# Optimization experiments

Hardware: AMD Instinct MI355X
Metric: run time of the kernel (lower is better)

The kernel has to match this reference:

```python
import jax, jax.numpy as jnp
from jax import lax
import numpy as np

B, T, H, I, O = 256, 2048, 150, 1, 1

def setup_inputs() -> dict:
    key = jax.random.key(0)
    ks = jax.random.split(key, 7)
    s = 1.0 / np.sqrt(H)
    return {
        "input": jax.random.normal(ks[0], (B, T), dtype=jnp.float32),
        "W_ih": jax.random.uniform(ks[1], (3 * H, I), jnp.float32, -s, s),
        "W_hh": jax.random.uniform(ks[2], (3 * H, H), jnp.float32, -s, s),
        "b_ih": jax.random.uniform(ks[3], (3 * H,), jnp.float32, -s, s),
        "b_hh": jax.random.uniform(ks[4], (3 * H,), jnp.float32, -s, s),
        "W_lin": jax.random.uniform(ks[5], (O, H), jnp.float32, -s, s),
        "b_lin": jax.random.uniform(ks[6], (O,), jnp.float32, -s, s),
    }

def reference(input, W_ih, W_hh, b_ih, b_hh, W_lin, b_lin):
    # input: [B, T]; GRUCell recurrence with relu on hidden, per-step linear head.
    hidden = W_hh.shape[1]

    def step(h, x_t):  # h: [B, H], x_t: [B, 1]
        gi = x_t @ W_ih.T + b_ih          # [B, 3H]
        gh = h @ W_hh.T + b_hh            # [B, 3H]
        i_r, i_z, i_n = jnp.split(gi, 3, axis=-1)
        h_r, h_z, h_n = jnp.split(gh, 3, axis=-1)
        r = jax.nn.sigmoid(i_r + h_r)
        z = jax.nn.sigmoid(i_z + h_z)
        n = jnp.tanh(i_n + r * h_n)
        h_new = jax.nn.relu((1.0 - z) * n + z * h)  # relu applied as in original
        y = h_new @ W_lin.T + b_lin       # [B, 1]
        return h_new, y

    xs = jnp.transpose(input)[:, :, None]            # [T, B, 1]
    h0 = jnp.zeros((input.shape[0], hidden), input.dtype)
    _, ys = lax.scan(step, h0, xs)                   # ys: [T, B, 1]
    return jnp.transpose(ys[:, :, 0])                # [B, T] (stack dim=1, squeeze(2))
```

## Files before the change

### kernel.cpp

```cpp
#include <hip/hip_runtime.h>
#include <math.h>


#define BB 256
#define TT 2048
#define HH 150
#define H3 450

typedef float fx2 __attribute__((ext_vector_type(2)));

#define WCLOB \
  "v100","v101","v102","v103","v104","v105","v106","v107","v108","v109", \
  "v110","v111","v112","v113","v114","v115","v116","v117","v118","v119", \
  "v120","v121","v122","v123","v124","v125","v126","v127","v128","v129", \
  "v130","v131","v132","v133","v134","v135","v136","v137","v138","v139", \
  "v140","v141","v142","v143","v144","v145","v146","v147","v148","v149", \
  "v150","v151","v152","v153","v154","v155","v156","v157","v158","v159", \
  "v160","v161","v162","v163","v164","v165","v166","v167","v168","v169", \
  "v170","v171","v172","v173","v174","v175","v176","v177","v178","v179", \
  "v180","v181","v182","v183","v184","v185","v186","v187","v188","v189", \
  "v190","v191","v192","v193","v194","v195","v196","v197","v198","v199", \
  "v200","v201","v202","v203","v204","v205","v206","v207","v208","v209", \
  "v210","v211","v212","v213","v214","v215","v216","v217","v218","v219", \
  "v220","v221","v222","v223","v224","v225","v226","v227","v228","v229", \
  "v230","v231","v232","v233","v234","v235","v236","v237","v238","v239", \
  "v240","v241","v242","v243","v244","v245","v246","v247","v248","v249", \
  "v250","v251"

#define LD8(a0,a1,b0,b1,c0,c1,d0,d1,OFF) \
  "global_load_dword v" #a0 ", %[p0], off offset:" #OFF "\n\t" \
  "global_load_dword v" #a1 ", %[p1], off offset:" #OFF "\n\t" \
  "global_load_dword v" #b0 ", %[p2], off offset:" #OFF "\n\t" \
  "global_load_dword v" #b1 ", %[p3], off offset:" #OFF "\n\t" \
  "global_load_dword v" #c0 ", %[p4], off offset:" #OFF "\n\t" \
  "global_load_dword v" #c1 ", %[p5], off offset:" #OFF "\n\t" \
  "global_load_dword v" #d0 ", %[p6], off offset:" #OFF "\n\t" \
  "global_load_dword v" #d1 ", %[p7], off offset:" #OFF "\n\t"

#define PKB(sp, vp, acc) \
  "v_pk_fma_f32 " acc ", " sp ", " vp ", " acc " op_sel:[0,0,0] op_sel_hi:[0,1,1]\n\t"

#define G4(m0,m1,m2,m3, A0,B0,C0,D0, A1,B1,C1,D1, A2,B2,C2,D2, A3,B3,C3,D3) \
  "v_readlane_b32 s20, %[hq], " #m0 "\n\t" \
  "v_readlane_b32 s22, %[hq], " #m1 "\n\t" \
  "v_readlane_b32 s24, %[hq], " #m2 "\n\t" \
  "v_readlane_b32 s26, %[hq], " #m3 "\n\t" \
  PKB("s[20:21]", A0, "%[a01]") PKB("s[20:21]", B0, "%[a23]") \
  PKB("s[20:21]", C0, "%[a45]") PKB("s[20:21]", D0, "%[a67]") \
  PKB("s[22:23]", A1, "%[a01]") PKB("s[22:23]", B1, "%[a23]") \
  PKB("s[22:23]", C1, "%[a45]") PKB("s[22:23]", D1, "%[a67]") \
  PKB("s[24:25]", A2, "%[a01]") PKB("s[24:25]", B2, "%[a23]") \
  PKB("s[24:25]", C2, "%[a45]") PKB("s[24:25]", D2, "%[a67]") \
  PKB("s[26:27]", A3, "%[a01]") PKB("s[26:27]", B3, "%[a23]") \
  PKB("s[26:27]", C3, "%[a45]") PKB("s[26:27]", D3, "%[a67]")

__global__ __launch_bounds__(512, 2) void gru_seq_kernel(
    const float* __restrict__ input,
    const float* __restrict__ W_ih,
    const float* __restrict__ W_hh,
    const float* __restrict__ b_ih,
    const float* __restrict__ b_hh,
    const float* __restrict__ W_lin,
    const float* __restrict__ b_lin,
    float* __restrict__ out)
{
    const int b    = blockIdx.x;
    const int tid  = threadIdx.x;
    const int lane = tid & 63;
    const int wid  = tid >> 6;

    __shared__ float xrow[TT];
    __shared__ float PPf[4160];
    __shared__ float hb[520];
    __shared__ float yout[TT];

    ((float4*)xrow)[tid] = ((const float4*)(input + (size_t)b * TT))[tid];
    hb[tid < 512 ? tid : 0] = 0.f;
    if (tid < 8) hb[512 + tid] = 0.f;

    const int r0 = 8 * lane;
#define ROWP(r) ((r) == H3 ? W_lin : W_hh + ((r) < H3 ? (r) : (H3 - 1)) * HH)
    const float* p0 = ROWP(r0)     + wid;
    const float* p1 = ROWP(r0 + 1) + wid;
    const float* p2 = ROWP(r0 + 2) + wid;
    const float* p3 = ROWP(r0 + 3) + wid;
    const float* p4 = ROWP(r0 + 4) + wid;
    const float* p5 = ROWP(r0 + 5) + wid;
    const float* p6 = ROWP(r0 + 6) + wid;
    const float* p7 = ROWP(r0 + 7) + wid;

    asm volatile(
        LD8(100,101,138,139,176,177,214,215, 0)
        LD8(102,103,140,141,178,179,216,217, 32)
        LD8(104,105,142,143,180,181,218,219, 64)
        LD8(106,107,144,145,182,183,220,221, 96)
        LD8(108,109,146,147,184,185,222,223, 128)
        LD8(110,111,148,149,186,187,224,225, 160)
        LD8(112,113,150,151,188,189,226,227, 192)
        LD8(114,115,152,153,190,191,228,229, 224)
        LD8(116,117,154,155,192,193,230,231, 256)
        LD8(118,119,156,157,194,195,232,233, 288)
        LD8(120,121,158,159,196,197,234,235, 320)
        LD8(122,123,160,161,198,199,236,237, 352)
        LD8(124,125,162,163,200,201,238,239, 384)
        LD8(126,127,164,165,202,203,240,241, 416)
        LD8(128,129,166,167,204,205,242,243, 448)
        LD8(130,131,168,169,206,207,244,245, 480)
        LD8(132,133,170,171,208,209,246,247, 512)
        LD8(134,135,172,173,210,211,248,249, 544)
        "s_waitcnt vmcnt(0)\n\t"
        :
        : [p0] "v"(p0), [p1] "v"(p1), [p2] "v"(p2), [p3] "v"(p3),
          [p4] "v"(p4), [p5] "v"(p5), [p6] "v"(p6), [p7] "v"(p7)
        : WCLOB, "memory");
    {
        const int t18 = (wid < 6) ? 144 : 136;
        float w0 = p0[t18], w1 = p1[t18], w2 = p2[t18], w3 = p3[t18];
        float w4 = p4[t18], w5 = p5[t18], w6 = p6[t18], w7 = p7[t18];
        asm volatile(
            "v_mov_b32 v136, %0\n\tv_mov_b32 v137, %1\n\t"
            "v_mov_b32 v174, %2\n\tv_mov_b32 v175, %3\n\t"
            "v_mov_b32 v212, %4\n\tv_mov_b32 v213, %5\n\t"
            "v_mov_b32 v250, %6\n\tv_mov_b32 v251, %7\n\t"
            :: "v"(w0), "v"(w1), "v"(w2), "v"(w3),
               "v"(w4), "v"(w5), "v"(w6), "v"(w7)
            : "v136","v137","v174","v175","v212","v213","v250","v251");
    }

    float wih_r = 0.f, wih_z = 0.f, wih_n = 0.f;
    float bih_r = 0.f, bih_z = 0.f, bih_n = 0.f;
    float bhh_r = 0.f, bhh_z = 0.f, bhh_n = 0.f;
    if (tid < HH) {
        wih_r = W_ih[tid];          bih_r = b_ih[tid];          bhh_r = b_hh[tid];
        wih_z = W_ih[HH + tid];     bih_z = b_ih[HH + tid];     bhh_z = b_hh[HH + tid];
        wih_n = W_ih[2 * HH + tid]; bih_n = b_ih[2 * HH + tid]; bhh_n = b_hh[2 * HH + tid];
    }
    const float blin = b_lin[0];
    float hreg = 0.f;
    float* outb = out + (size_t)b * TT;
    float2* st = (float2*)PPf + wid * 260 + lane;
    int ir = 0, iz = 0, in_ = 0;
    if (tid < HH) {
        int r;
        r = tid;        ir  = (((r & 7) >> 1) * 65 + (r >> 3)) * 2 + (r & 1);
        r = HH + tid;   iz  = (((r & 7) >> 1) * 65 + (r >> 3)) * 2 + (r & 1);
        r = 2*HH + tid; in_ = (((r & 7) >> 1) * 65 + (r >> 3)) * 2 + (r & 1);
    }
    const int iy = (1 * 65 + 56) * 2;

    __syncthreads();

    for (int t = 0; t <= TT; ++t) {
        float hq = hb[wid * 65 + lane];
        fx2 a01; a01.x = 0.f; a01.y = 0.f;
        fx2 a23; a23.x = 0.f; a23.y = 0.f;
        fx2 a45; a45.x = 0.f; a45.y = 0.f;
        fx2 a67; a67.x = 0.f; a67.y = 0.f;
        asm volatile(
            G4( 0, 1, 2, 3,
                "v[100:101]","v[138:139]","v[176:177]","v[214:215]",
                "v[102:103]","v[140:141]","v[178:179]","v[216:217]",
                "v[104:105]","v[142:143]","v[180:181]","v[218:219]",
                "v[106:107]","v[144:145]","v[182:183]","v[220:221]")
            G4( 4, 5, 6, 7,
                "v[108:109]","v[146:147]","v[184:185]","v[222:223]",
                "v[110:111]","v[148:149]","v[186:187]","v[224:225]",
                "v[112:113]","v[150:151]","v[188:189]","v[226:227]",
                "v[114:115]","v[152:153]","v[190:191]","v[228:229]")
            G4( 8, 9,10,11,
                "v[116:117]","v[154:155]","v[192:193]","v[230:231]",
                "v[118:119]","v[156:157]","v[194:195]","v[232:233]",
                "v[120:121]","v[158:159]","v[196:197]","v[234:235]",
                "v[122:123]","v[160:161]","v[198:199]","v[236:237]")
            G4(12,13,14,15,
                "v[124:125]","v[162:163]","v[200:201]","v[238:239]",
                "v[126:127]","v[164:165]","v[202:203]","v[240:241]",
                "v[128:129]","v[166:167]","v[204:205]","v[242:243]",
                "v[130:131]","v[168:169]","v[206:207]","v[244:245]")
            "v_readlane_b32 s28, %[hq], 16\n\t"
            "v_readlane_b32 s30, %[hq], 17\n\t"
            "v_readlane_b32 s20, %[hq], 18\n\t"
            PKB("s[28:29]", "v[132:133]", "%[a01]")
            PKB("s[28:29]", "v[170:171]", "%[a23]")
            PKB("s[28:29]", "v[208:209]", "%[a45]")
            PKB("s[28:29]", "v[246:247]", "%[a67]")
            PKB("s[30:31]", "v[134:135]", "%[a01]")
            PKB("s[30:31]", "v[172:173]", "%[a23]")
            PKB("s[30:31]", "v[210:211]", "%[a45]")
            PKB("s[30:31]", "v[248:249]", "%[a67]")
            PKB("s[20:21]", "v[136:137]", "%[a01]")
            PKB("s[20:21]", "v[174:175]", "%[a23]")
            PKB("s[20:21]", "v[212:213]", "%[a45]")
            PKB("s[20:21]", "v[250:251]", "%[a67]")
            : [a01] "+v"(a01), [a23] "+v"(a23),
              [a45] "+v"(a45), [a67] "+v"(a67)
            : [hq] "v"(hq)
            : "s20","s22","s24","s26","s28","s30", WCLOB);
        float2 s01; s01.x = a01.x; s01.y = a01.y;
        float2 s23; s23.x = a23.x; s23.y = a23.y;
        float2 s45; s45.x = a45.x; s45.y = a45.y;
        float2 s67; s67.x = a67.x; s67.y = a67.y;
        st[0]   = s01;
        st[65]  = s23;
        st[130] = s45;
        st[195] = s67;
        __syncthreads();

        if (t < TT && tid < HH) {
            float x  = xrow[t];
            float pr = (((PPf[ir]         + PPf[ir + 520])
                       + (PPf[ir + 1040]  + PPf[ir + 1560]))
                      + ((PPf[ir + 2080]  + PPf[ir + 2600])
                       + (PPf[ir + 3120]  + PPf[ir + 3640]))) + bhh_r;
            float pz = (((PPf[iz]         + PPf[iz + 520])
                       + (PPf[iz + 1040]  + PPf[iz + 1560]))
                      + ((PPf[iz + 2080]  + PPf[iz + 2600])
                       + (PPf[iz + 3120]  + PPf[iz + 3640]))) + bhh_z;
            float pn = (((PPf[in_]        + PPf[in_ + 520])
                       + (PPf[in_ + 1040] + PPf[in_ + 1560]))
                      + ((PPf[in_ + 2080] + PPf[in_ + 2600])
                       + (PPf[in_ + 3120] + PPf[in_ + 3640]))) + bhh_n;
            float gr = fmaf(x, wih_r, bih_r) + pr;
            float gz = fmaf(x, wih_z, bih_z) + pz;
            float r  = 1.f / (1.f + __expf(-gr));
            float z  = 1.f / (1.f + __expf(-gz));
            float ta = fmaf(x, wih_n, bih_n) + r * pn;
            ta = fminf(fmaxf(ta, -15.f), 15.f);
            float e  = __expf(2.f * ta);
            float n  = (e - 1.f) / (e + 1.f);
            float hnew = fmaf(z, hreg - n, n);
            hnew = fmaxf(hnew, 0.f);
            hreg = hnew;
            hb[(tid & 7) * 65 + (tid >> 3)] = hnew;
        }
        if (t > 0 && tid == H3) {
            yout[t - 1] = (((PPf[iy]        + PPf[iy + 520])
                          + (PPf[iy + 1040] + PPf[iy + 1560]))
                         + ((PPf[iy + 2080] + PPf[iy + 2600])
                          + (PPf[iy + 3120] + PPf[iy + 3640]))) + blin;
        }
        __syncthreads();
    }

    ((float4*)outb)[tid] = ((const float4*)yout)[tid];
}

extern "C" void kernel_launch(void* const* d_in, const int* in_sizes, int n_in,
                              void* d_out, int out_size, void* d_ws, size_t ws_size,
                              hipStream_t stream) {
    const float* input = (const float*)d_in[0];
    const float* W_ih  = (const float*)d_in[1];
    const float* W_hh  = (const float*)d_in[2];
    const float* b_ih  = (const float*)d_in[3];
    const float* b_hh  = (const float*)d_in[4];
    const float* W_lin = (const float*)d_in[5];
    const float* b_lin = (const float*)d_in[6];
    float* out = (float*)d_out;

    gru_seq_kernel<<<dim3(BB), dim3(512), 0, stream>>>(
        input, W_ih, W_hh, b_ih, b_hh, W_lin, b_lin, out);
}
```

Before: 1.881 ms.

## Keep hidden state in registers and double-buffer partial sums to halve barriers

Each hidden unit is now owned by the lane and wave that already broadcasts it through readlane. The new state stays in the `hq` register instead of going through a shared `hb` buffer. The partial-sum buffer is split into two alternating copies, so each timestep needs one `__syncthreads` instead of two. This also spreads the gate math across all eight waves instead of the first three. The cost is twice the shared memory for partial sums and an unrolled-by-two loop.

Result: slower. 2.198 ms (+16.8%).

```diff
diff --git a/kernel.cpp b/kernel.cpp
--- a/kernel.cpp
+++ b/kernel.cpp
@@ -54,6 +54,48 @@
   PKB("s[26:27]", A3, "%[a01]") PKB("s[26:27]", B3, "%[a23]") \
   PKB("s[26:27]", C3, "%[a45]") PKB("s[26:27]", D3, "%[a67]")
 
+#define P1ASM(a01v, a23v, a45v, a67v, hqv) \
+    asm volatile( \
+        G4( 0, 1, 2, 3, \
+            "v[100:101]","v[138:139]","v[176:177]","v[214:215]", \
+            "v[102:103]","v[140:141]","v[178:179]","v[216:217]", \
+            "v[104:105]","v[142:143]","v[180:181]","v[218:219]", \
+            "v[106:107]","v[144:145]","v[182:183]","v[220:221]") \
+        G4( 4, 5, 6, 7, \
+            "v[108:109]","v[146:147]","v[184:185]","v[222:223]", \
+            "v[110:111]","v[148:149]","v[186:187]","v[224:225]", \
+            "v[112:113]","v[150:151]","v[188:189]","v[226:227]", \
+            "v[114:115]","v[152:153]","v[190:191]","v[228:229]") \
+        G4( 8, 9,10,11, \
+            "v[116:117]","v[154:155]","v[192:193]","v[230:231]", \
+            "v[118:119]","v[156:157]","v[194:195]","v[232:233]", \
+            "v[120:121]","v[158:159]","v[196:197]","v[234:235]", \
+            "v[122:123]","v[160:161]","v[198:199]","v[236:237]") \
+        G4(12,13,14,15, \
+            "v[124:125]","v[162:163]","v[200:201]","v[238:239]", \
+            "v[126:127]","v[164:165]","v[202:203]","v[240:241]", \
+            "v[128:129]","v[166:167]","v[204:205]","v[242:243]", \
+            "v[130:131]","v[168:169]","v[206:207]","v[244:245]") \
+        "v_readlane_b32 s28, %[hq], 16\n\t" \
+        "v_readlane_b32 s30, %[hq], 17\n\t" \
+        "v_readlane_b32 s20, %[hq], 18\n\t" \
+        PKB("s[28:29]", "v[132:133]", "%[a01]") \
+        PKB("s[28:29]", "v[170:171]", "%[a23]") \
+        PKB("s[28:29]", "v[208:209]", "%[a45]") \
+        PKB("s[28:29]", "v[246:247]", "%[a67]") \
+        PKB("s[30:31]", "v[134:135]", "%[a01]") \
+        PKB("s[30:31]", "v[172:173]", "%[a23]") \
+        PKB("s[30:31]", "v[210:211]", "%[a45]") \
+        PKB("s[30:31]", "v[248:249]", "%[a67]") \
+        PKB("s[20:21]", "v[136:137]", "%[a01]") \
+        PKB("s[20:21]", "v[174:175]", "%[a23]") \
+        PKB("s[20:21]", "v[212:213]", "%[a45]") \
+        PKB("s[20:21]", "v[250:251]", "%[a67]") \
+        : [a01] "+v"(a01v), [a23] "+v"(a23v), \
+          [a45] "+v"(a45v), [a67] "+v"(a67v) \
+        : [hq] "v"(hqv) \
+        : "s20","s22","s24","s26","s28","s30", WCLOB)
+
 __global__ __launch_bounds__(512, 2) void gru_seq_kernel(
     const float* __restrict__ input,
     const float* __restrict__ W_ih,
@@ -70,13 +112,11 @@
     const int wid  = tid >> 6;
 
     __shared__ float xrow[TT];
-    __shared__ float PPf[4160];
-    __shared__ float hb[520];
+    __shared__ float PPfA[4160];
+    __shared__ float PPfB[4160];
     __shared__ float yout[TT];
 
     ((float4*)xrow)[tid] = ((const float4*)(input + (size_t)b * TT))[tid];
-    hb[tid < 512 ? tid : 0] = 0.f;
-    if (tid < 8) hb[512 + tid] = 0.f;
 
     const int r0 = 8 * lane;
 #define ROWP(r) ((r) == H3 ? W_lin : W_hh + ((r) < H3 ? (r) : (H3 - 1)) * HH)
@@ -127,75 +167,43 @@
             : "v136","v137","v174","v175","v212","v213","v250","v251");
     }
 
+    const int  u    = 8 * lane + wid;
+    const bool pact = (lane < 19) && (u < HH);
+    const bool yw   = (wid == 6) && (lane == 18);
+
     float wih_r = 0.f, wih_z = 0.f, wih_n = 0.f;
     float bih_r = 0.f, bih_z = 0.f, bih_n = 0.f;
     float bhh_r = 0.f, bhh_z = 0.f, bhh_n = 0.f;
-    if (tid < HH) {
-        wih_r = W_ih[tid];          bih_r = b_ih[tid];          bhh_r = b_hh[tid];
-        wih_z = W_ih[HH + tid];     bih_z = b_ih[HH + tid];     bhh_z = b_hh[HH + tid];
-        wih_n = W_ih[2 * HH + tid]; bih_n = b_ih[2 * HH + tid]; bhh_n = b_hh[2 * HH + tid];
+    if (pact) {
+        wih_r = W_ih[u];          bih_r = b_ih[u];          bhh_r = b_hh[u];
+        wih_z = W_ih[HH + u];     bih_z = b_ih[HH + u];     bhh_z = b_hh[HH + u];
+        wih_n = W_ih[2 * HH + u]; bih_n = b_ih[2 * HH + u]; bhh_n = b_hh[2 * HH + u];
     }
     const float blin = b_lin[0];
-    float hreg = 0.f;
     float* outb = out + (size_t)b * TT;
-    float2* st = (float2*)PPf + wid * 260 + lane;
+
+    float2* stA = (float2*)PPfA + wid * 260 + lane;
+    float2* stB = (float2*)PPfB + wid * 260 + lane;
+
     int ir = 0, iz = 0, in_ = 0;
-    if (tid < HH) {
+    if (pact) {
         int r;
-        r = tid;        ir  = (((r & 7) >> 1) * 65 + (r >> 3)) * 2 + (r & 1);
-        r = HH + tid;   iz  = (((r & 7) >> 1) * 65 + (r >> 3)) * 2 + (r & 1);
-        r = 2*HH + tid; in_ = (((r & 7) >> 1) * 65 + (r >> 3)) * 2 + (r & 1);
+        r = u;          ir  = (((r & 7) >> 1) * 65 + (r >> 3)) * 2 + (r & 1);
+        r = HH + u;     iz  = (((r & 7) >> 1) * 65 + (r >> 3)) * 2 + (r & 1);
+        r = 2*HH + u;   in_ = (((r & 7) >> 1) * 65 + (r >> 3)) * 2 + (r & 1);
     }
     const int iy = (1 * 65 + 56) * 2;
 
+    float hq = 0.f;
+
     __syncthreads();
 
-    for (int t = 0; t <= TT; ++t) {
-        float hq = hb[wid * 65 + lane];
+    auto step = [&](float2* st, const float* pb, int t) {
         fx2 a01; a01.x = 0.f; a01.y = 0.f;
         fx2 a23; a23.x = 0.f; a23.y = 0.f;
         fx2 a45; a45.x = 0.f; a45.y = 0.f;
         fx2 a67; a67.x = 0.f; a67.y = 0.f;
-        asm volatile(
-            G4( 0, 1, 2, 3,
-                "v[100:101]","v[138:139]","v[176:177]","v[214:215]",
-                "v[102:103]","v[140:141]","v[178:179]","v[216:217]",
-                "v[104:105]","v[142:143]","v[180:181]","v[218:219]",
-                "v[106:107]","v[144:145]","v[182:183]","v[220:221]")
-            G4( 4, 5, 6, 7,
-                "v[108:109]","v[146:147]","v[184:185]","v[222:223]",
-                "v[110:111]","v[148:149]","v[186:187]","v[224:225]",
-                "v[112:113]","v[150:151]","v[188:189]","v[226:227]",
-                "v[114:115]","v[152:153]","v[190:191]","v[228:229]")
-            G4( 8, 9,10,11,
-                "v[116:117]","v[154:155]","v[192:193]","v[230:231]",
-                "v[118:119]","v[156:157]","v[194:195]","v[232:233]",
-                "v[120:121]","v[158:159]","v[196:197]","v[234:235]",
-                "v[122:123]","v[160:161]","v[198:199]","v[236:237]")
-            G4(12,13,14,15,
-                "v[124:125]","v[162:163]","v[200:201]","v[238:239]",
-                "v[126:127]","v[164:165]","v[202:203]","v[240:241]",
-                "v[128:129]","v[166:167]","v[204:205]","v[242:243]",
-                "v[130:131]","v[168:169]","v[206:207]","v[244:245]")
-            "v_readlane_b32 s28, %[hq], 16\n\t"
-            "v_readlane_b32 s30, %[hq], 17\n\t"
-            "v_readlane_b32 s20, %[hq], 18\n\t"
-            PKB("s[28:29]", "v[132:133]", "%[a01]")
-            PKB("s[28:29]", "v[170:171]", "%[a23]")
-            PKB("s[28:29]", "v[208:209]", "%[a45]")
-            PKB("s[28:29]", "v[246:247]", "%[a67]")
-            PKB("s[30:31]", "v[134:135]", "%[a01]")
-            PKB("s[30:31]", "v[172:173]", "%[a23]")
-            PKB("s[30:31]", "v[210:211]", "%[a45]")
-            PKB("s[30:31]", "v[248:249]", "%[a67]")
-            PKB("s[20:21]", "v[136:137]", "%[a01]")
-            PKB("s[20:21]", "v[174:175]", "%[a23]")
-            PKB("s[20:21]", "v[212:213]", "%[a45]")
-            PKB("s[20:21]", "v[250:251]", "%[a67]")
-            : [a01] "+v"(a01), [a23] "+v"(a23),
-              [a45] "+v"(a45), [a67] "+v"(a67)
-            : [hq] "v"(hq)
-            : "s20","s22","s24","s26","s28","s30", WCLOB);
+        P1ASM(a01, a23, a45, a67, hq);
         float2 s01; s01.x = a01.x; s01.y = a01.y;
         float2 s23; s23.x = a23.x; s23.y = a23.y;
         float2 s45; s45.x = a45.x; s45.y = a45.y;
@@ -205,21 +213,20 @@
         st[130] = s45;
         st[195] = s67;
         __syncthreads();
-
-        if (t < TT && tid < HH) {
+        if (pact && t < TT) {
             float x  = xrow[t];
-            float pr = (((PPf[ir]         + PPf[ir + 520])
-                       + (PPf[ir + 1040]  + PPf[ir + 1560]))
-                      + ((PPf[ir + 2080]  + PPf[ir + 2600])
-                       + (PPf[ir + 3120]  + PPf[ir + 3640]))) + bhh_r;
-            float pz = (((PPf[iz]         + PPf[iz + 520])
-                       + (PPf[iz + 1040]  + PPf[iz + 1560]))
-                      + ((PPf[iz + 2080]  + PPf[iz + 2600])
-                       + (PPf[iz + 3120]  + PPf[iz + 3640]))) + bhh_z;
-            float pn = (((PPf[in_]        + PPf[in_ + 520])
-                       + (PPf[in_ + 1040] + PPf[in_ + 1560]))
-                      + ((PPf[in_ + 2080] + PPf[in_ + 2600])
-                       + (PPf[in_ + 3120] + PPf[in_ + 3640]))) + bhh_n;
+            float pr = (((pb[ir]         + pb[ir + 520])
+                       + (pb[ir + 1040]  + pb[ir + 1560]))
+                      + ((pb[ir + 2080]  + pb[ir + 2600])
+                       + (pb[ir + 3120]  + pb[ir + 3640]))) + bhh_r;
+            float pz = (((pb[iz]         + pb[iz + 520])
+                       + (pb[iz + 1040]  + pb[iz + 1560]))
+                      + ((pb[iz + 2080]  + pb[iz + 2600])
+                       + (pb[iz + 3120]  + pb[iz + 3640]))) + bhh_z;
+            float pn = (((pb[in_]        + pb[in_ + 520])
+                       + (pb[in_ + 1040] + pb[in_ + 1560]))
+                      + ((pb[in_ + 2080] + pb[in_ + 2600])
+                       + (pb[in_ + 3120] + pb[in_ + 3640]))) + bhh_n;
             float gr = fmaf(x, wih_r, bih_r) + pr;
             float gz = fmaf(x, wih_z, bih_z) + pz;
             float r  = 1.f / (1.f + __expf(-gr));
@@ -228,20 +235,24 @@
             ta = fminf(fmaxf(ta, -15.f), 15.f);
             float e  = __expf(2.f * ta);
             float n  = (e - 1.f) / (e + 1.f);
-            float hnew = fmaf(z, hreg - n, n);
-            hnew = fmaxf(hnew, 0.f);
-            hreg = hnew;
-            hb[(tid & 7) * 65 + (tid >> 3)] = hnew;
+            float hnew = fmaf(z, hq - n, n);
+            hq = fmaxf(hnew, 0.f);
         }
-        if (t > 0 && tid == H3) {
-            yout[t - 1] = (((PPf[iy]        + PPf[iy + 520])
-                          + (PPf[iy + 1040] + PPf[iy + 1560]))
-                         + ((PPf[iy + 2080] + PPf[iy + 2600])
-                          + (PPf[iy + 3120] + PPf[iy + 3640]))) + blin;
+        if (yw && t > 0) {
+            yout[t - 1] = (((pb[iy]        + pb[iy + 520])
+                          + (pb[iy + 1040] + pb[iy + 1560]))
+                         + ((pb[iy + 2080] + pb[iy + 2600])
+                          + (pb[iy + 3120] + pb[iy + 3640]))) + blin;
         }
-        __syncthreads();
-    }
-
+    };
+
+    for (int t = 0; t < TT; t += 2) {
+        step(stA, PPfA, t);
+        step(stB, PPfB, t + 1);
+    }
+    step(stA, PPfA, TT);
+
+    __syncthreads();
     ((float4*)outb)[tid] = ((const float4*)yout)[tid];
 }
 
```
